# Kernel tuning notes

Measured on AMD Instinct MI355X. Metric: run time of the kernel, lower is better.

Reference implementation:

```python
import jax, jax.numpy as jnp
import numpy as np
from jax import lax

SIGMA = 2.0
RADIUS = 8  # int(truncate(4.0)*sigma + 0.5) per scipy gaussian_filter

_x = np.arange(-RADIUS, RADIUS + 1, dtype=np.float32)
_gw = np.exp(-0.5 * (_x / SIGMA) ** 2)
GAUSS_W = jnp.asarray(_gw / _gw.sum(), dtype=jnp.float32)  # 17 taps, sums to 1
DERIV_W = jnp.asarray([-1.0, 0.0, 1.0], dtype=jnp.float32)   # scipy correlate1d [-1,0,1]
SMOOTH_W = jnp.asarray([1.0, 2.0, 1.0], dtype=jnp.float32)

DN = ('NCHW', 'OIHW', 'NCHW')

def _corr_h(img, w, pad_mode):
    # 1D cross-correlation along H axis of [B,1,H,W]
    r = w.shape[0] // 2
    p = jnp.pad(img, ((0, 0), (0, 0), (r, r), (0, 0)), mode=pad_mode)
    k = w.reshape(1, 1, -1, 1)
    return lax.conv_general_dilated(p, k, (1, 1), 'VALID', dimension_numbers=DN)

def _corr_w(img, w, pad_mode):
    # 1D cross-correlation along W axis of [B,1,H,W]
    r = w.shape[0] // 2
    p = jnp.pad(img, ((0, 0), (0, 0), (0, 0), (r, r)), mode=pad_mode)
    k = w.reshape(1, 1, 1, -1)
    return lax.conv_general_dilated(p, k, (1, 1), 'VALID', dimension_numbers=DN)

def setup_inputs() -> dict:
    key = jax.random.key(0)
    x = jax.random.normal(key, (32, 3, 512, 512), dtype=jnp.float32)
    return {"x": x}

def reference(x) -> jnp.ndarray:
    # channel mean -> [B,1,H,W]
    g = jnp.mean(x, axis=1, keepdims=True)
    # gaussian blur, scipy mode='reflect' == numpy/jnp 'symmetric' padding
    blur = _corr_w(_corr_h(g, GAUSS_W, 'symmetric'), GAUSS_W, 'symmetric')
    # scipy sobel, mode='constant' (zero pad): deriv along given axis, [1,2,1] smooth along other
    sx = _corr_w(_corr_h(blur, DERIV_W, 'constant'), SMOOTH_W, 'constant')  # axis=0 (H)
    sy = _corr_h(_corr_w(blur, DERIV_W, 'constant'), SMOOTH_W, 'constant')  # axis=1 (W)
    return jnp.hypot(sx, sy)  # [B,1,H,W]
```

## Files before the change

### kernel.cpp

```cpp
#include <hip/hip_runtime.h>
#include <math.h>

#define TILE 64
#define HALO 9
#define REG  (TILE + 2*HALO)
#define REGS 84
#define BR   (TILE + 2)
#define BRS  68
#define IMG  512

__device__ __forceinline__ int reflect_idx(int i) {
    if (i < 0) i = -i - 1;
    if (i >= IMG) i = 2 * IMG - 1 - i;
    return i;
}

__global__ __launch_bounds__(256) void sobel_fused(
    const float* __restrict__ x, float* __restrict__ out)
{
    __shared__ float sA[REG * REGS];
    __shared__ float sB[BR * REGS];

    const int t  = threadIdx.x;
    const int w0 = blockIdx.x * TILE;
    const int h0 = blockIdx.y * TILE;
    const int b  = blockIdx.z;

    float gw[17];
    {
        float s = 0.f;
        #pragma unroll
        for (int i = 0; i < 17; ++i) {
            float xx = (float)(i - 8);
            gw[i] = expf(-0.125f * xx * xx);
            s += gw[i];
        }
        float inv = 1.0f / s;
        #pragma unroll
        for (int i = 0; i < 17; ++i) gw[i] *= inv;
    }

    const float* xb = x + (size_t)b * 3 * IMG * IMG;
    const float third = 1.0f / 3.0f;
    for (int idx = t; idx < REG * REG; idx += 256) {
        int r = idx / REG, c = idx - r * REG;
        int gr = reflect_idx(h0 - HALO + r);
        int gc = reflect_idx(w0 - HALO + c);
        const float* p = xb + gr * IMG + gc;
        sA[r * REGS + c] = (p[0] + p[IMG * IMG] + p[2 * IMG * IMG]) * third;
    }
    __syncthreads();

    for (int idx = t; idx < BR * REG; idx += 256) {
        int r = idx / REG, c = idx - r * REG;
        float acc = 0.f;
        #pragma unroll
        for (int k = 0; k < 17; ++k) acc += gw[k] * sA[(r + k) * REGS + c];
        sB[r * REGS + c] = acc;
    }
    __syncthreads();

    float* sBlur = sA;
    for (int idx = t; idx < BR * BR; idx += 256) {
        int r = idx / BR, c = idx - r * BR;
        float acc = 0.f;
        #pragma unroll
        for (int k = 0; k < 17; ++k) acc += gw[k] * sB[r * REGS + c + k];
        int gr = h0 - 1 + r, gc = w0 - 1 + c;
        bool in = (gr >= 0) & (gr < IMG) & (gc >= 0) & (gc < IMG);
        sBlur[r * BRS + c] = in ? acc : 0.f;
    }
    __syncthreads();

    for (int idx = t; idx < TILE * TILE; idx += 256) {
        int r = idx >> 6, c = idx & 63;
        const float* bp = sBlur + r * BRS + c;
        float tl = bp[0],       tm = bp[1],       tr = bp[2];
        float ml = bp[BRS],                        mr = bp[BRS + 2];
        float bl = bp[2 * BRS], bm = bp[2 * BRS + 1], br2 = bp[2 * BRS + 2];
        float sx = (bl - tl) + 2.f * (bm - tm) + (br2 - tr);
        float sy = (tr - tl) + 2.f * (mr - ml) + (br2 - bl);
        out[((size_t)b * IMG + (h0 + r)) * IMG + (w0 + c)] = sqrtf(sx * sx + sy * sy);
    }
}

extern "C" void kernel_launch(void* const* d_in, const int* in_sizes, int n_in,
                              void* d_out, int out_size, void* d_ws, size_t ws_size,
                              hipStream_t stream) {
    const float* x = (const float*)d_in[0];
    float* out = (float*)d_out;
    dim3 grid(IMG / TILE, IMG / TILE, 32);
    dim3 block(256);
    hipLaunchKernelGGL(sobel_fused, grid, block, 0, stream, x, out);
}
```

Measured before the change: 186.0 us.

## Register-block separable Gaussian passes and Sobel stencil to cut LDS reads

Each thread now computes 22 consecutive outputs of the vertical and horizontal Gaussian passes. It keeps running accumulators in registers, so every loaded LDS value is reused across up to 17 taps instead of being reloaded per tap. The Sobel stage processes 4 rows per thread using a 6x3 register window. Shared-memory strides change to 85 to reduce bank conflicts. The cost is much higher register pressure (22 accumulators plus 17 weights) and some idle threads, since only 246 and 198 of 256 threads work in the blur passes.

```diff
diff --git a/kernel.cpp b/kernel.cpp
--- a/kernel.cpp
+++ b/kernel.cpp
@@ -1,13 +1,14 @@
 #include <hip/hip_runtime.h>
 #include <math.h>
 
-#define TILE 64
-#define HALO 9
-#define REG  (TILE + 2*HALO)
-#define REGS 84
-#define BR   (TILE + 2)
-#define BRS  68
-#define IMG  512
+#define IMG   512
+#define TILE  64
+#define HALO  9
+#define AROWS 82
+#define ASTR  85
+#define BROWS 66
+#define BSTR  85
+#define CSTR  68
 
 __device__ __forceinline__ int reflect_idx(int i) {
     if (i < 0) i = -i - 1;
@@ -18,8 +19,8 @@
 __global__ __launch_bounds__(256) void sobel_fused(
     const float* __restrict__ x, float* __restrict__ out)
 {
-    __shared__ float sA[REG * REGS];
-    __shared__ float sB[BR * REGS];
+    __shared__ float sA[AROWS * ASTR];
+    __shared__ float sB[BROWS * BSTR];
 
     const int t  = threadIdx.x;
     const int w0 = blockIdx.x * TILE;
@@ -42,45 +43,89 @@
 
     const float* xb = x + (size_t)b * 3 * IMG * IMG;
     const float third = 1.0f / 3.0f;
-    for (int idx = t; idx < REG * REG; idx += 256) {
-        int r = idx / REG, c = idx - r * REG;
+    for (int idx = t; idx < AROWS * AROWS; idx += 256) {
+        int r = idx / AROWS, c = idx - r * AROWS;
         int gr = reflect_idx(h0 - HALO + r);
         int gc = reflect_idx(w0 - HALO + c);
         const float* p = xb + gr * IMG + gc;
-        sA[r * REGS + c] = (p[0] + p[IMG * IMG] + p[2 * IMG * IMG]) * third;
+        sA[r * ASTR + c] = (p[0] + p[IMG * IMG] + p[2 * IMG * IMG]) * third;
     }
     __syncthreads();
 
-    for (int idx = t; idx < BR * REG; idx += 256) {
-        int r = idx / REG, c = idx - r * REG;
-        float acc = 0.f;
+    if (t < 246) {
+        int c   = t % 82;
+        int seg = t / 82;
+        int r0  = seg * 22;
+        float acc[22];
         #pragma unroll
-        for (int k = 0; k < 17; ++k) acc += gw[k] * sA[(r + k) * REGS + c];
-        sB[r * REGS + c] = acc;
+        for (int j = 0; j < 22; ++j) acc[j] = 0.f;
+        #pragma unroll
+        for (int i = 0; i < 38; ++i) {
+            float v = sA[(r0 + i) * ASTR + c];
+            #pragma unroll
+            for (int j = 0; j < 22; ++j) {
+                int k = i - j;
+                if (k >= 0 && k < 17) acc[j] += gw[k] * v;
+            }
+        }
+        #pragma unroll
+        for (int j = 0; j < 22; ++j) sB[(r0 + j) * BSTR + c] = acc[j];
     }
     __syncthreads();
 
-    float* sBlur = sA;
-    for (int idx = t; idx < BR * BR; idx += 256) {
-        int r = idx / BR, c = idx - r * BR;
-        float acc = 0.f;
+    float* sC = sA;
+    if (t < 198) {
+        int r   = t % 66;
+        int seg = t / 66;
+        int c0  = seg * 22;
+        float acc[22];
         #pragma unroll
-        for (int k = 0; k < 17; ++k) acc += gw[k] * sB[r * REGS + c + k];
-        int gr = h0 - 1 + r, gc = w0 - 1 + c;
-        bool in = (gr >= 0) & (gr < IMG) & (gc >= 0) & (gc < IMG);
-        sBlur[r * BRS + c] = in ? acc : 0.f;
+        for (int j = 0; j < 22; ++j) acc[j] = 0.f;
+        #pragma unroll
+        for (int i = 0; i < 38; ++i) {
+            float v = sB[r * BSTR + c0 + i];
+            #pragma unroll
+            for (int j = 0; j < 22; ++j) {
+                int k = i - j;
+                if (k >= 0 && k < 17) acc[j] += gw[k] * v;
+            }
+        }
+        int gr = h0 - 1 + r;
+        #pragma unroll
+        for (int j = 0; j < 22; ++j) {
+            int c  = c0 + j;
+            int gc = w0 - 1 + c;
+            bool in = (gr >= 0) & (gr < IMG) & (gc >= 0) & (gc < IMG);
+            sC[r * CSTR + c] = in ? acc[j] : 0.f;
+        }
     }
     __syncthreads();
 
-    for (int idx = t; idx < TILE * TILE; idx += 256) {
-        int r = idx >> 6, c = idx & 63;
-        const float* bp = sBlur + r * BRS + c;
-        float tl = bp[0],       tm = bp[1],       tr = bp[2];
-        float ml = bp[BRS],                        mr = bp[BRS + 2];
-        float bl = bp[2 * BRS], bm = bp[2 * BRS + 1], br2 = bp[2 * BRS + 2];
-        float sx = (bl - tl) + 2.f * (bm - tm) + (br2 - tr);
-        float sy = (tr - tl) + 2.f * (mr - ml) + (br2 - bl);
-        out[((size_t)b * IMG + (h0 + r)) * IMG + (w0 + c)] = sqrtf(sx * sx + sy * sy);
+    {
+        int c  = t & 63;
+        int rq = t >> 6;
+        #pragma unroll
+        for (int it = 0; it < 4; ++it) {
+            int r0 = (rq + it * 4) * 4;
+            const float* bp = sC + r0 * CSTR + c;
+            float m[6][3];
+            #pragma unroll
+            for (int rr = 0; rr < 6; ++rr) {
+                #pragma unroll
+                for (int cc = 0; cc < 3; ++cc)
+                    m[rr][cc] = bp[rr * CSTR + cc];
+            }
+            #pragma unroll
+            for (int dr = 0; dr < 4; ++dr) {
+                float tl = m[dr][0],   tm = m[dr][1],   tr = m[dr][2];
+                float ml = m[dr+1][0],                  mr = m[dr+1][2];
+                float bl = m[dr+2][0], bm = m[dr+2][1], br2 = m[dr+2][2];
+                float sx = (bl - tl) + 2.f * (bm - tm) + (br2 - tr);
+                float sy = (tr - tl) + 2.f * (mr - ml) + (br2 - bl);
+                out[((size_t)b * IMG + (h0 + r0 + dr)) * IMG + (w0 + c)]
+                    = sqrtf(sx * sx + sy * sy);
+            }
+        }
     }
 }
 
```

After: 191.3 us. 1.03x slower.
